# Kernel optimization log

Hardware: AMD Instinct MI355X
Metric: run time of the kernel (lower is better)

Reference implementation:

```python
import jax, jax.numpy as jnp
import numpy as np

N = 50000
E0 = 800000
IN_CH = 128
HID = 64
OUT_CH = 64
HEADS = 2
NEG_SLOPE = 0.2


def _xavier(key, shape):
    fan_in, fan_out = shape[-2], shape[-1]
    limit = (6.0 / (fan_in + fan_out)) ** 0.5
    return jax.random.uniform(key, shape, jnp.float32, -limit, limit)


def setup_inputs() -> dict:
    key = jax.random.key(0)
    ks = jax.random.split(key, 10)
    x = jax.random.normal(ks[0], (N, IN_CH), jnp.float32)
    src = jax.random.randint(ks[1], (E0,), 0, N)
    dst = jax.random.randint(ks[2], (E0,), 0, N)
    dst = jnp.where(src == dst, (dst + 1) % N, dst)  # no self loops in input
    edge_index = jnp.stack([src, dst]).astype(jnp.int64)
    emb_w = _xavier(ks[3], (HID, IN_CH))
    emb_b = jnp.zeros((HID,), jnp.float32)
    # layer 0: in=HID, out=HID, heads=HEADS
    w0 = _xavier(ks[4], (HEADS, HID, HID))
    a0 = _xavier(ks[5], (1, HEADS, 2 * HID))
    # layer 1: in=HEADS*HID, out=HID, heads=HEADS
    w1 = _xavier(ks[6], (HEADS, HEADS * HID, HID))
    a1 = _xavier(ks[7], (1, HEADS, 2 * HID))
    # layer 2: in=HEADS*HID, out=OUT_CH, heads=1, concat=False
    w2 = _xavier(ks[8], (1, HEADS * HID, OUT_CH))
    a2 = _xavier(ks[9], (1, 1, 2 * OUT_CH))
    return {"x": x, "edge_index": edge_index, "emb_w": emb_w, "emb_b": emb_b,
            "w0": w0, "a0": a0, "w1": w1, "a1": a1, "w2": w2, "a2": a2}


def gat_layer(x, w, a, src, dst, concat):
    # x: [N, F_in]; w: [H, F_in, C]; a: [1, H, 2C]; src/dst: [E]
    C = w.shape[-1]
    xh = jnp.einsum('nf,hfc->nhc', x, w)               # [N, H, C]
    a_i, a_j = a[0, :, :C], a[0, :, C:]                # each [H, C]
    # (cat(x_i, x_j) * a).sum(-1) == <x_i, a_i> + <x_j, a_j>; compute per node then gather
    s_i = jnp.einsum('nhc,hc->nh', xh, a_i)            # [N, H]
    s_j = jnp.einsum('nhc,hc->nh', xh, a_j)            # [N, H]
    alpha = jax.nn.leaky_relu(s_i[dst] + s_j[src], NEG_SLOPE)  # [E, H]
    # segment softmax over destination nodes
    m = jax.ops.segment_max(alpha, dst, num_segments=N)
    alpha = jnp.exp(alpha - m[dst])
    denom = jax.ops.segment_sum(alpha, dst, num_segments=N)
    alpha = alpha / (denom[dst] + 1e-16)
    out = jax.ops.segment_sum(xh[src] * alpha[:, :, None], dst, num_segments=N)  # [N, H, C]
    if concat:
        return out.reshape(N, -1)
    return out.mean(axis=1)


def _forward(x, edge_index, emb_w, emb_b, w0, a0, w1, a1, w2, a2):
    # add self loops (inputs contain none, matching remove+add in the source)
    loop = jnp.arange(N, dtype=edge_index.dtype)
    src = jnp.concatenate([edge_index[0], loop])
    dst = jnp.concatenate([edge_index[1], loop])
    h = x @ emb_w.T + emb_b                            # nn.Linear embedding
    h = jax.nn.elu(gat_layer(h, w0, a0, src, dst, True))
    h = jax.nn.elu(gat_layer(h, w1, a1, src, dst, True))
    h = jax.nn.elu(gat_layer(h, w2, a2, src, dst, False))
    return h


def reference(x, edge_index, emb_w, emb_b, w0, a0, w1, a1, w2, a2):
    return _forward(x, edge_index, emb_w, emb_b, w0, a0, w1, a1, w2, a2)
```

## Files before the change

kernel.cpp:

```cpp
#include <hip/hip_runtime.h>
#include <math.h>

typedef __attribute__((ext_vector_type(8))) short short8v;
typedef __attribute__((ext_vector_type(4))) float float4v;

union uf32 { unsigned int u; float f; };

__device__ __forceinline__ unsigned short f2b(float f) {
  uf32 v; v.f = f;
  unsigned int u = v.u;
  return (unsigned short)((u + 0x7fffu + ((u >> 16) & 1u)) >> 16);
}


__global__ void hist8(const int* __restrict__ ei, int* __restrict__ cnt8,
                      unsigned short* __restrict__ lpos, int E0, int N) {
  int e = blockIdx.x * 256 + threadIdx.x;
  if (e >= E0 + N) return;
  int vx = blockIdx.x & 7;
  int d = (e < E0) ? ei[E0 + e] : (e - E0);
  lpos[e] = (unsigned short)atomicAdd(&cnt8[vx * N + d], 1);
}

__global__ void fold8(const int* __restrict__ cnt8, int* __restrict__ base8,
                      int* __restrict__ cnt, int* __restrict__ part, int N) {
  __shared__ int lds[256];
  int d = blockIdx.x * 256 + threadIdx.x;
  int run = 0;
  if (d < N) {
#pragma unroll
    for (int x = 0; x < 8; ++x) {
      int t = cnt8[x * N + d];
      base8[x * N + d] = run;
      run += t;
    }
    cnt[d] = run;
  }
  lds[threadIdx.x] = (d < N) ? run : 0;
  __syncthreads();
  for (int o = 128; o; o >>= 1) {
    if (threadIdx.x < o) lds[threadIdx.x] += lds[threadIdx.x + o];
    __syncthreads();
  }
  if (threadIdx.x == 0) part[blockIdx.x] = lds[0];
}

__global__ void scan_carry(int* __restrict__ part, int nb) {
  __shared__ int lds[256];
  __shared__ int carry;
  if (threadIdx.x == 0) carry = 0;
  __syncthreads();
  for (int t0 = 0; t0 < nb; t0 += 256) {
    int t = t0 + threadIdx.x;
    int v = (t < nb) ? part[t] : 0;
    lds[threadIdx.x] = v;
    __syncthreads();
    for (int o = 1; o < 256; o <<= 1) {
      int x = (threadIdx.x >= o) ? lds[threadIdx.x - o] : 0;
      __syncthreads();
      lds[threadIdx.x] += x;
      __syncthreads();
    }
    if (t < nb) part[t] = carry + lds[threadIdx.x] - v;
    __syncthreads();
    if (threadIdx.x == 255) carry += lds[255];
    __syncthreads();
  }
}

__global__ void scan3(const int* __restrict__ cnt, const int* __restrict__ part,
                      const int* __restrict__ base8, int* __restrict__ rp,
                      int* __restrict__ rb8, int N, int E) {
  __shared__ int lds[256];
  int t = threadIdx.x;
  int idx = blockIdx.x * 256 + t;
  int v = (idx < N) ? cnt[idx] : 0;
  lds[t] = v;
  __syncthreads();
  for (int o = 1; o < 256; o <<= 1) {
    int x = (t >= o) ? lds[t - o] : 0;
    __syncthreads();
    lds[t] += x;
    __syncthreads();
  }
  if (idx < N) {
    const int rpv = part[blockIdx.x] + lds[t] - v;
    rp[idx] = rpv;
#pragma unroll
    for (int x = 0; x < 8; ++x) rb8[x * N + idx] = rpv + base8[x * N + idx];
  }
  if (blockIdx.x == 0 && t == 0) rp[N] = E;
}

__global__ void setup_kernel(int* __restrict__ cnt8, int nz, int gZ,
                             const float* __restrict__ emb_w, const float* __restrict__ w0,
                             const float* __restrict__ w1, const float* __restrict__ w2,
                             unsigned short* __restrict__ pE, unsigned short* __restrict__ p0,
                             unsigned short* __restrict__ p1, unsigned short* __restrict__ p2) {
  if ((int)blockIdx.x < gZ) {
    int i = blockIdx.x * 256 + threadIdx.x;
    if (i < nz) cnt8[i] = 0;
    return;
  }
  int b = blockIdx.x - gZ;
  const float* w; unsigned short* bp;
  int F, sf, sc, h;
  if (b < 32)       { w = emb_w; bp = pE; F = 128; sf = 1;  sc = 128; h = 0; }
  else if (b < 64)  { b -= 32;  w = w0; bp = p0; F = 64;  sf = 64; sc = 1; h = b / 16; b %= 16; }
  else if (b < 128) { b -= 64;  w = w1; bp = p1; F = 128; sf = 64; sc = 1; h = b / 32; b %= 32; }
  else              { b -= 128; w = w2; bp = p2; F = 128; sf = 64; sc = 1; h = 0; }
  int i = b * 256 + threadIdx.x;
  if (i >= F * 64) return;
  int j = i & 7, colc = (i >> 3) & 15, g = (i >> 7) & 3, ct = (i >> 9) & 3, kk = i >> 11;
  int f = kk * 32 + g * 8 + j;
  int c = ct * 16 + colc;
  float v = w[(size_t)h * F * 64 + (size_t)f * sf + (size_t)c * sc];
  bp[(size_t)h * F * 64 + i] = f2b(v);
}

__global__ __launch_bounds__(256) void fill_emb_l0(
    const int* __restrict__ ei, const int* __restrict__ rb8,
    const unsigned short* __restrict__ lpos, int* __restrict__ col,
    int E0, int N, int gR,
    const float* __restrict__ x, const unsigned short* __restrict__ packE,
    const float* __restrict__ emb_b, const unsigned short* __restrict__ pack0,
    const float* __restrict__ a0, unsigned short* __restrict__ xhb,
    float* __restrict__ si, float* __restrict__ sj) {
  constexpr int SA = 136;
  constexpr int SB = 72;
  __shared__ __align__(16) unsigned short lds[64 * SA];

  if ((int)blockIdx.x >= gR) {
    const int e = (blockIdx.x - gR) * 256 + threadIdx.x;
    if (e >= E0 + N) return;
    const int vx = (e >> 8) & 7;
    int s, d;
    if (e < E0) { s = ei[e]; d = ei[E0 + e]; }
    else        { s = e - E0; d = s; }
    col[rb8[vx * N + d] + lpos[e]] = s;
    return;
  }

  const int nrows = N;
  const int tid = threadIdx.x;
  const int lane = tid & 63;
  const int wv = tid >> 6;
  const int n0 = blockIdx.x * 64;

#pragma unroll
  for (int i0 = 0; i0 < 64 * 32; i0 += 256) {
    const int i = i0 + tid;
    const int row = i >> 5, c4 = i & 31;
    int rg = n0 + row;
    if (rg >= nrows) rg = nrows - 1;
    const float4 v = *reinterpret_cast<const float4*>(x + (size_t)rg * 128 + c4 * 4);
    unsigned short* d = lds + row * SA + c4 * 4;
    d[0] = f2b(v.x); d[1] = f2b(v.y); d[2] = f2b(v.z); d[3] = f2b(v.w);
  }
  __syncthreads();

  const int g = lane >> 4;
  const int cl = lane & 15;

  short8v xf[4];
  {
    const unsigned short* ar = lds + (wv * 16 + cl) * SA + g * 8;
#pragma unroll
    for (int kk = 0; kk < 4; ++kk) xf[kk] = *reinterpret_cast<const short8v*>(ar + kk * 32);
  }

  float4v eacc[4];
#pragma unroll
  for (int ct = 0; ct < 4; ++ct) eacc[ct] = (float4v){0.f, 0.f, 0.f, 0.f};
#pragma unroll
  for (int kk = 0; kk < 4; ++kk) {
#pragma unroll
    for (int ct = 0; ct < 4; ++ct) {
      const short8v bf = *reinterpret_cast<const short8v*>(
          packE + ((size_t)((kk * 4 + ct) * 4 + g)) * 128 + cl * 8);
      eacc[ct] = __builtin_amdgcn_mfma_f32_16x16x32_bf16(xf[kk], bf, eacc[ct], 0, 0, 0);
    }
  }
  __syncthreads();

#pragma unroll
  for (int ct = 0; ct < 4; ++ct) {
    const float b = emb_b[ct * 16 + cl];
#pragma unroll
    for (int reg = 0; reg < 4; ++reg) {
      const int row = wv * 16 + g * 4 + reg;
      lds[row * SB + ct * 16 + cl] = f2b(eacc[ct][reg] + b);
    }
  }
  __syncthreads();

  short8v af[2];
  {
    const unsigned short* ar2 = lds + (wv * 16 + cl) * SB + g * 8;
#pragma unroll
    for (int kk = 0; kk < 2; ++kk) af[kk] = *reinterpret_cast<const short8v*>(ar2 + kk * 32);
  }

#pragma unroll
  for (int h = 0; h < 2; ++h) {
    const unsigned short* __restrict__ bph = pack0 + (size_t)h * (64 * 64);

    float4v acc[4];
#pragma unroll
    for (int ct = 0; ct < 4; ++ct) acc[ct] = (float4v){0.f, 0.f, 0.f, 0.f};
#pragma unroll
    for (int kk = 0; kk < 2; ++kk) {
#pragma unroll
      for (int ct = 0; ct < 4; ++ct) {
        const short8v bf = *reinterpret_cast<const short8v*>(
            bph + ((size_t)((kk * 4 + ct) * 4 + g)) * 128 + cl * 8);
        acc[ct] = __builtin_amdgcn_mfma_f32_16x16x32_bf16(af[kk], bf, acc[ct], 0, 0, 0);
      }
    }

#pragma unroll
    for (int ct = 0; ct < 4; ++ct) {
      const int c = ct * 16 + cl;
#pragma unroll
      for (int reg = 0; reg < 4; ++reg) {
        const int n = n0 + wv * 16 + g * 4 + reg;
        if (n < nrows) xhb[(size_t)n * 128 + h * 64 + c] = f2b(acc[ct][reg]);
      }
    }

    float pi[4] = {0.f, 0.f, 0.f, 0.f}, pj[4] = {0.f, 0.f, 0.f, 0.f};
#pragma unroll
    for (int ct = 0; ct < 4; ++ct) {
      const float av = a0[h * 128 + ct * 16 + cl];
      const float bv = a0[h * 128 + 64 + ct * 16 + cl];
#pragma unroll
      for (int reg = 0; reg < 4; ++reg) {
        pi[reg] = fmaf(acc[ct][reg], av, pi[reg]);
        pj[reg] = fmaf(acc[ct][reg], bv, pj[reg]);
      }
    }
#pragma unroll
    for (int reg = 0; reg < 4; ++reg) {
#pragma unroll
      for (int o = 8; o; o >>= 1) {
        pi[reg] += __shfl_xor(pi[reg], o, 64);
        pj[reg] += __shfl_xor(pj[reg], o, 64);
      }
    }
    if (cl == 0) {
#pragma unroll
      for (int reg = 0; reg < 4; ++reg) {
        const int n = n0 + wv * 16 + g * 4 + reg;
        if (n < nrows) {
          si[(size_t)n * 2 + h] = pi[reg];
          sj[(size_t)n * 2 + h] = pj[reg];
        }
      }
    }
  }
}

template <int F, int H, bool SCORES, bool OBF>
__global__ __launch_bounds__(256) void gemm_mfma(
    const unsigned short* __restrict__ in, const unsigned short* __restrict__ bp,
    const float* __restrict__ a, void* __restrict__ xh_out,
    float* __restrict__ si, float* __restrict__ sj, int nrows) {
  constexpr int SA = F + 8;
  constexpr int NK = F / 32;
  constexpr int HC = H * 64;
  __shared__ __align__(16) unsigned short A_lds[64 * SA];

  const int tid = threadIdx.x;
  const int lane = tid & 63;
  const int wv = tid >> 6;
  const int n0 = blockIdx.x * 64;

  {
    constexpr int NCH = 64 * F / 8;
#pragma unroll
    for (int i0 = 0; i0 < NCH; i0 += 256) {
      const int i = i0 + tid;
      const int row = i / (F / 8);
      const int c8 = i % (F / 8);
      int rg = n0 + row;
      if (rg >= nrows) rg = nrows - 1;
      const short8v v = *reinterpret_cast<const short8v*>(in + (size_t)rg * F + c8 * 8);
      *reinterpret_cast<short8v*>(A_lds + row * SA + c8 * 8) = v;
    }
  }
  __syncthreads();

  const int g = lane >> 4;
  const int cl = lane & 15;

  short8v af[NK];
  const unsigned short* ar = A_lds + (wv * 16 + cl) * SA + g * 8;
#pragma unroll
  for (int kk = 0; kk < NK; ++kk) af[kk] = *reinterpret_cast<const short8v*>(ar + kk * 32);

#pragma unroll
  for (int h = 0; h < H; ++h) {
    const unsigned short* __restrict__ bph = bp + (size_t)h * (F * 64);

    float4v acc[4];
#pragma unroll
    for (int ct = 0; ct < 4; ++ct) acc[ct] = (float4v){0.f, 0.f, 0.f, 0.f};

#pragma unroll
    for (int kk = 0; kk < NK; ++kk) {
#pragma unroll
      for (int ct = 0; ct < 4; ++ct) {
        const short8v bf = *reinterpret_cast<const short8v*>(
            bph + ((size_t)((kk * 4 + ct) * 4 + g)) * 128 + cl * 8);
        acc[ct] = __builtin_amdgcn_mfma_f32_16x16x32_bf16(af[kk], bf, acc[ct], 0, 0, 0);
      }
    }

#pragma unroll
    for (int ct = 0; ct < 4; ++ct) {
      const int c = ct * 16 + cl;
#pragma unroll
      for (int reg = 0; reg < 4; ++reg) {
        const int n = n0 + wv * 16 + g * 4 + reg;
        if (n < nrows) {
          const size_t idx = (size_t)n * HC + h * 64 + c;
          if (OBF) ((unsigned short*)xh_out)[idx] = f2b(acc[ct][reg]);
          else     ((float*)xh_out)[idx] = acc[ct][reg];
        }
      }
    }

    if (SCORES) {
      float pi[4] = {0.f, 0.f, 0.f, 0.f}, pj[4] = {0.f, 0.f, 0.f, 0.f};
#pragma unroll
      for (int ct = 0; ct < 4; ++ct) {
        const float av = a[h * 128 + ct * 16 + cl];
        const float bv = a[h * 128 + 64 + ct * 16 + cl];
#pragma unroll
        for (int reg = 0; reg < 4; ++reg) {
          pi[reg] = fmaf(acc[ct][reg], av, pi[reg]);
          pj[reg] = fmaf(acc[ct][reg], bv, pj[reg]);
        }
      }
#pragma unroll
      for (int reg = 0; reg < 4; ++reg) {
#pragma unroll
        for (int o = 8; o; o >>= 1) {
          pi[reg] += __shfl_xor(pi[reg], o, 64);
          pj[reg] += __shfl_xor(pj[reg], o, 64);
        }
      }
      if (cl == 0) {
#pragma unroll
        for (int reg = 0; reg < 4; ++reg) {
          const int n = n0 + wv * 16 + g * 4 + reg;
          if (n < nrows) {
            si[(size_t)n * H + h] = pi[reg];
            sj[(size_t)n * H + h] = pj[reg];
          }
        }
      }
    }
  }
}

template <int H, bool OBF>
__global__ __launch_bounds__(256) void agg_kernel(
    const unsigned short* __restrict__ xh, const float* __restrict__ si_g,
    const float* __restrict__ sj_g, const int* __restrict__ rp,
    const int* __restrict__ col, void* __restrict__ out, int N) {
  constexpr int HC = H * 64;
  const int lane = threadIdx.x & 63;
  const int n = blockIdx.x * 4 + (threadIdx.x >> 6);
  if (n >= N) return;
  const int el = lane & 31;
  const int hl = (H == 2) ? (lane >> 5) : 0;

  const int base = rp[n];
  const int deg = rp[n + 1] - base;
  const float siv = si_g[(size_t)n * H + hl];

  const int soff = (H == 1) ? (lane >> 5) : 0;
  const int qoff = (H == 1) ? (lane >> 5) : (lane & 32);
  constexpr int STEP = (H == 2) ? 1 : 2;
  const unsigned int loff = (H == 2) ? (unsigned)lane * 2 : (unsigned)el * 2;

  float m = 0.f, den = 0.f, acc0 = 0.f, acc1 = 0.f;

  for (int start = 0; start < deg; start += 32) {
    const int k = start + el;
    const bool vld = k < deg;
    const int s = vld ? col[base + k] : 0;
    float al = -INFINITY;
    if (vld) {
      const float t = siv + sj_g[(size_t)s * H + hl];
      al = (t > 0.f) ? t : 0.2f * t;
    }
    float cm = al;
#pragma unroll
    for (int o = 16; o; o >>= 1) cm = fmaxf(cm, __shfl_xor(cm, o, 64));
    if (start == 0) {
      m = cm;
    } else {
      const float nm = fmaxf(m, cm);
      const float r = __expf(m - nm);
      den *= r; acc0 *= r; acc1 *= r; m = nm;
    }
    const float p = vld ? __expf(al - m) : 0.f;
    float ps = p;
#pragma unroll
    for (int o = 16; o; o >>= 1) ps += __shfl_xor(ps, o, 64);
    den += ps;

    const int cc = min(32, deg - start);
    int kk = 0;
    for (; kk + 8 * STEP <= cc; kk += 8 * STEP) {
      int sb[8]; float qb[8]; unsigned int uv[8];
#pragma unroll
      for (int u = 0; u < 8; ++u) {
        const int e = kk + u * STEP;
        sb[u] = __shfl(s, e + soff, 64);
        qb[u] = __shfl(p, e + qoff, 64);
      }
#pragma unroll
      for (int u = 0; u < 8; ++u)
        uv[u] = *reinterpret_cast<const unsigned int*>(xh + (size_t)sb[u] * HC + loff);
#pragma unroll
      for (int u = 0; u < 8; ++u) {
        uf32 lo, hi;
        lo.u = uv[u] << 16;
        hi.u = uv[u] & 0xffff0000u;
        acc0 = fmaf(qb[u], lo.f, acc0);
        acc1 = fmaf(qb[u], hi.f, acc1);
      }
    }
    for (; kk + 4 * STEP <= cc; kk += 4 * STEP) {
      int sb[4]; float qb[4]; unsigned int uv[4];
#pragma unroll
      for (int u = 0; u < 4; ++u) {
        const int e = kk + u * STEP;
        sb[u] = __shfl(s, e + soff, 64);
        qb[u] = __shfl(p, e + qoff, 64);
      }
#pragma unroll
      for (int u = 0; u < 4; ++u)
        uv[u] = *reinterpret_cast<const unsigned int*>(xh + (size_t)sb[u] * HC + loff);
#pragma unroll
      for (int u = 0; u < 4; ++u) {
        uf32 lo, hi;
        lo.u = uv[u] << 16;
        hi.u = uv[u] & 0xffff0000u;
        acc0 = fmaf(qb[u], lo.f, acc0);
        acc1 = fmaf(qb[u], hi.f, acc1);
      }
    }
    for (; kk < cc; kk += STEP) {
      const int sb = __shfl(s, kk + soff, 64);
      const float qb = __shfl(p, kk + qoff, 64);
      const unsigned int uv = *reinterpret_cast<const unsigned int*>(xh + (size_t)sb * HC + loff);
      uf32 lo, hi;
      lo.u = uv << 16;
      hi.u = uv & 0xffff0000u;
      acc0 = fmaf(qb, lo.f, acc0);
      acc1 = fmaf(qb, hi.f, acc1);
    }
  }

  if (H == 2) {
    const float invd = 1.f / (den + 1e-16f);
    float v0 = acc0 * invd, v1 = acc1 * invd;
    v0 = (v0 > 0.f) ? v0 : expm1f(v0);
    v1 = (v1 > 0.f) ? v1 : expm1f(v1);
    if (OBF) {
      unsigned int pk = ((unsigned int)f2b(v1) << 16) | (unsigned int)f2b(v0);
      *reinterpret_cast<unsigned int*>((unsigned short*)out + (size_t)n * 128 + lane * 2) = pk;
    } else {
      float2 o; o.x = v0; o.y = v1;
      *reinterpret_cast<float2*>((float*)out + (size_t)n * 128 + lane * 2) = o;
    }
  } else {
    acc0 += __shfl_xor(acc0, 32, 64);
    acc1 += __shfl_xor(acc1, 32, 64);
    if (lane < 32) {
      const float invd = 1.f / (den + 1e-16f);
      float v0 = acc0 * invd, v1 = acc1 * invd;
      v0 = (v0 > 0.f) ? v0 : expm1f(v0);
      v1 = (v1 > 0.f) ? v1 : expm1f(v1);
      if (OBF) {
        unsigned int pk = ((unsigned int)f2b(v1) << 16) | (unsigned int)f2b(v0);
        *reinterpret_cast<unsigned int*>((unsigned short*)out + (size_t)n * 64 + el * 2) = pk;
      } else {
        float2 o; o.x = v0; o.y = v1;
        *reinterpret_cast<float2*>((float*)out + (size_t)n * 64 + el * 2) = o;
      }
    }
  }
}

extern "C" void kernel_launch(void* const* d_in, const int* in_sizes, int n_in,
                              void* d_out, int out_size, void* d_ws, size_t ws_size,
                              hipStream_t stream) {
  const float* x     = (const float*)d_in[0];
  const int*   ei    = (const int*)d_in[1];
  const float* emb_w = (const float*)d_in[2];
  const float* emb_b = (const float*)d_in[3];
  const float* w0    = (const float*)d_in[4];
  const float* a0    = (const float*)d_in[5];
  const float* w1    = (const float*)d_in[6];
  const float* a1    = (const float*)d_in[7];
  const float* w2    = (const float*)d_in[8];
  const float* a2    = (const float*)d_in[9];

  const int IN_CH = 128;
  int N  = in_sizes[0] / IN_CH;
  int E0 = in_sizes[1] / 2;
  int E  = E0 + N;

  char* p = (char*)d_ws;
  auto alloc = [&](size_t bytes) -> char* {
    char* r = p;
    p += (bytes + 255) & ~(size_t)255;
    return r;
  };
  unsigned short* hA  = (unsigned short*)alloc((size_t)N * 128 * 2);
  unsigned short* hB  = (unsigned short*)alloc((size_t)N * 128 * 2);
  unsigned short* xhb = (unsigned short*)alloc((size_t)N * 128 * 2);
  float* si   = (float*)alloc((size_t)N * 2 * 4);
  float* sj   = (float*)alloc((size_t)N * 2 * 4);
  unsigned short* packE = (unsigned short*)alloc(128 * 64 * 2);
  unsigned short* pack0 = (unsigned short*)alloc(2 * 64 * 64 * 2);
  unsigned short* pack1 = (unsigned short*)alloc(2 * 128 * 64 * 2);
  unsigned short* pack2 = (unsigned short*)alloc(128 * 64 * 2);
  int* rp    = (int*)alloc((size_t)(N + 1) * 4);
  int* cnt   = (int*)alloc((size_t)N * 4);
  int* cnt8  = (int*)alloc((size_t)8 * N * 4);
  int* base8 = (int*)alloc((size_t)8 * N * 4);
  int* rb8   = (int*)alloc((size_t)8 * N * 4);
  unsigned short* lpos = (unsigned short*)alloc((size_t)E * 2);
  int* col   = (int*)alloc((size_t)E * 4);
  int* part  = (int*)alloc(1024);

  dim3 blk(256);
  int gN = (N + 255) / 256;
  int gE = (E + 255) / 256;
  int gZ = (8 * N + 255) / 256;
  int gR = (N + 63) / 64;

  setup_kernel<<<gZ + 160, blk, 0, stream>>>(cnt8, 8 * N, gZ,
                                             emb_w, w0, w1, w2,
                                             packE, pack0, pack1, pack2);
  hist8<<<gE, blk, 0, stream>>>(ei, cnt8, lpos, E0, N);
  fold8<<<gN, blk, 0, stream>>>(cnt8, base8, cnt, part, N);
  scan_carry<<<1, blk, 0, stream>>>(part, gN);
  scan3<<<gN, blk, 0, stream>>>(cnt, part, base8, rp, rb8, N, E);

  fill_emb_l0<<<gR + gE, blk, 0, stream>>>(ei, rb8, lpos, col, E0, N, gR,
                                           x, packE, emb_b, pack0, a0, xhb, si, sj);
  agg_kernel<2, true><<<(N + 3) / 4, blk, 0, stream>>>(xhb, si, sj, rp, col, hB, N);

  gemm_mfma<128, 2, true, true><<<gR, blk, 0, stream>>>(hB, pack1, a1, xhb, si, sj, N);
  agg_kernel<2, true><<<(N + 3) / 4, blk, 0, stream>>>(xhb, si, sj, rp, col, hA, N);

  gemm_mfma<128, 1, true, true><<<gR, blk, 0, stream>>>(hA, pack2, a2, xhb, si, sj, N);
  agg_kernel<1, false><<<(N + 3) / 4, blk, 0, stream>>>(xhb, si, sj, rp, col, (float*)d_out, N);
}
```

Measured before the change: 193.4 us.

## Fuse three-kernel CSR row-pointer scan into single decoupled look-back scan

Replaces the fold8, scan_carry and scan3 kernels with one scan_fused kernel that uses per-block flags and a decoupled look-back to get each block's exclusive prefix. This drops two kernel launches, the serial single-block carry scan, and the intermediate cnt/base8/part buffers. Per-node bucket bases now stay in registers, and the flags share the cnt8 buffer so they are zeroed by setup_kernel. The look-back relies on blocks being scheduled roughly in order and on spin-waiting, and it uses relaxed atomics with 24-bit packed sums.

```diff
diff --git a/kernel.cpp b/kernel.cpp
--- a/kernel.cpp
+++ b/kernel.cpp
@@ -22,60 +22,67 @@
   lpos[e] = (unsigned short)atomicAdd(&cnt8[vx * N + d], 1);
 }
 
-__global__ void fold8(const int* __restrict__ cnt8, int* __restrict__ base8,
-                      int* __restrict__ cnt, int* __restrict__ part, int N) {
+__global__ __launch_bounds__(256) void scan_fused(
+    const int* __restrict__ cnt8, int* __restrict__ rp, int* __restrict__ rb8,
+    unsigned int* __restrict__ flags, int N, int E) {
   __shared__ int lds[256];
-  int d = blockIdx.x * 256 + threadIdx.x;
+  __shared__ int s_excl;
+  const int b = blockIdx.x;
+  const int t = threadIdx.x;
+  const int d = b * 256 + t;
+
   int run = 0;
+  int b8[8];
   if (d < N) {
 #pragma unroll
     for (int x = 0; x < 8; ++x) {
-      int t = cnt8[x * N + d];
-      base8[x * N + d] = run;
-      run += t;
-    }
-    cnt[d] = run;
-  }
-  lds[threadIdx.x] = (d < N) ? run : 0;
+      b8[x] = run;
+      run += cnt8[x * N + d];
+    }
+  }
+
+  lds[t] = (d < N) ? run : 0;
   __syncthreads();
   for (int o = 128; o; o >>= 1) {
-    if (threadIdx.x < o) lds[threadIdx.x] += lds[threadIdx.x + o];
+    if (t < o) lds[t] += lds[t + o];
     __syncthreads();
   }
-  if (threadIdx.x == 0) part[blockIdx.x] = lds[0];
-}
-
-__global__ void scan_carry(int* __restrict__ part, int nb) {
-  __shared__ int lds[256];
-  __shared__ int carry;
-  if (threadIdx.x == 0) carry = 0;
-  __syncthreads();
-  for (int t0 = 0; t0 < nb; t0 += 256) {
-    int t = t0 + threadIdx.x;
-    int v = (t < nb) ? part[t] : 0;
-    lds[threadIdx.x] = v;
-    __syncthreads();
-    for (int o = 1; o < 256; o <<= 1) {
-      int x = (threadIdx.x >= o) ? lds[threadIdx.x - o] : 0;
-      __syncthreads();
-      lds[threadIdx.x] += x;
-      __syncthreads();
-    }
-    if (t < nb) part[t] = carry + lds[threadIdx.x] - v;
-    __syncthreads();
-    if (threadIdx.x == 255) carry += lds[255];
-    __syncthreads();
-  }
-}
-
-__global__ void scan3(const int* __restrict__ cnt, const int* __restrict__ part,
-                      const int* __restrict__ base8, int* __restrict__ rp,
-                      int* __restrict__ rb8, int N, int E) {
-  __shared__ int lds[256];
-  int t = threadIdx.x;
-  int idx = blockIdx.x * 256 + t;
-  int v = (idx < N) ? cnt[idx] : 0;
-  lds[t] = v;
+  const int aggregate = lds[0];
+  if (t == 0)
+    __hip_atomic_store(&flags[b], (1u << 24) | (unsigned)aggregate,
+                       __ATOMIC_RELAXED, __HIP_MEMORY_SCOPE_AGENT);
+  __syncthreads();
+
+  if (t < 64) {
+    int excl = 0;
+    int wstart = b - 1;
+    while (wstart >= 0) {
+      const int myb = wstart - t;
+      unsigned v = 0;
+      if (myb >= 0) {
+        do {
+          v = __hip_atomic_load(&flags[myb], __ATOMIC_RELAXED, __HIP_MEMORY_SCOPE_AGENT);
+        } while ((v >> 24) == 0u);
+      }
+      const unsigned long long pm = __ballot(myb >= 0 && (v >> 24) == 2u);
+      const int firstP = pm ? (__ffsll((long long)pm) - 1) : 64;
+      int c = (myb >= 0 && t <= firstP) ? (int)(v & 0xFFFFFFu) : 0;
+#pragma unroll
+      for (int o = 32; o; o >>= 1) c += __shfl_xor(c, o, 64);
+      excl += c;
+      if (firstP < 64) break;
+      wstart -= 64;
+    }
+    if (t == 0) {
+      s_excl = excl;
+      __hip_atomic_store(&flags[b], (2u << 24) | (unsigned)(excl + aggregate),
+                         __ATOMIC_RELAXED, __HIP_MEMORY_SCOPE_AGENT);
+    }
+  }
+  __syncthreads();
+  const int excl = s_excl;
+
+  lds[t] = (d < N) ? run : 0;
   __syncthreads();
   for (int o = 1; o < 256; o <<= 1) {
     int x = (t >= o) ? lds[t - o] : 0;
@@ -83,13 +90,13 @@
     lds[t] += x;
     __syncthreads();
   }
-  if (idx < N) {
-    const int rpv = part[blockIdx.x] + lds[t] - v;
-    rp[idx] = rpv;
-#pragma unroll
-    for (int x = 0; x < 8; ++x) rb8[x * N + idx] = rpv + base8[x * N + idx];
-  }
-  if (blockIdx.x == 0 && t == 0) rp[N] = E;
+  if (d < N) {
+    const int rpv = excl + lds[t] - run;
+    rp[d] = rpv;
+#pragma unroll
+    for (int x = 0; x < 8; ++x) rb8[x * N + d] = rpv + b8[x];
+  }
+  if (b == 0 && t == 0) rp[N] = E;
 }
 
 __global__ void setup_kernel(int* __restrict__ cnt8, int nz, int gZ,
@@ -532,27 +539,23 @@
   unsigned short* pack1 = (unsigned short*)alloc(2 * 128 * 64 * 2);
   unsigned short* pack2 = (unsigned short*)alloc(128 * 64 * 2);
   int* rp    = (int*)alloc((size_t)(N + 1) * 4);
-  int* cnt   = (int*)alloc((size_t)N * 4);
-  int* cnt8  = (int*)alloc((size_t)8 * N * 4);
-  int* base8 = (int*)alloc((size_t)8 * N * 4);
+  int* cnt8  = (int*)alloc((size_t)(8 * N + 256) * 4);
+  unsigned int* flags = (unsigned int*)(cnt8 + 8 * N);
   int* rb8   = (int*)alloc((size_t)8 * N * 4);
   unsigned short* lpos = (unsigned short*)alloc((size_t)E * 2);
   int* col   = (int*)alloc((size_t)E * 4);
-  int* part  = (int*)alloc(1024);
 
   dim3 blk(256);
   int gN = (N + 255) / 256;
   int gE = (E + 255) / 256;
-  int gZ = (8 * N + 255) / 256;
+  int gZ = (8 * N + 256 + 255) / 256;
   int gR = (N + 63) / 64;
 
-  setup_kernel<<<gZ + 160, blk, 0, stream>>>(cnt8, 8 * N, gZ,
+  setup_kernel<<<gZ + 160, blk, 0, stream>>>(cnt8, 8 * N + 256, gZ,
                                              emb_w, w0, w1, w2,
                                              packE, pack0, pack1, pack2);
   hist8<<<gE, blk, 0, stream>>>(ei, cnt8, lpos, E0, N);
-  fold8<<<gN, blk, 0, stream>>>(cnt8, base8, cnt, part, N);
-  scan_carry<<<1, blk, 0, stream>>>(part, gN);
-  scan3<<<gN, blk, 0, stream>>>(cnt, part, base8, rp, rb8, N, E);
+  scan_fused<<<gN, blk, 0, stream>>>(cnt8, rp, rb8, flags, N, E);
 
   fill_emb_l0<<<gR + gE, blk, 0, stream>>>(ei, rb8, lpos, col, E0, N, gR,
                                            x, packE, emb_b, pack0, a0, xhb, si, sj);
```

After: 192.5 us. No clear change (-0.5%).
